# Kernel tuning notes

Measured on AMD Instinct MI355X. Metric: run time of the kernel, lower is better.

Reference implementation:

```python
import jax, jax.numpy as jnp
import numpy as np

N = 50000
K_CLASSES = 40
SIGMA = 0.2


def _lin(x, W, b):
    # x: [..., in], W: [out, in], b: [out]
    return x @ W.T + b


def setup_inputs() -> dict:
    key = jax.random.key(0)
    ks = iter(jax.random.split(key, 64))

    def rn(shape, scale=0.05):
        return jax.random.normal(next(ks), shape, dtype=jnp.float32) * scale

    inp = {
        "centre": jax.random.normal(next(ks), (N, 3), dtype=jnp.float32),
        "corner": jax.random.normal(next(ks), (N, 9), dtype=jnp.float32),
        "normal": jax.random.normal(next(ks), (N, 3), dtype=jnp.float32),
        "neighbour": jax.random.randint(next(ks), (N, 3), 0, N, dtype=jnp.int64 if jax.config.read('jax_enable_x64') else jnp.int32),
        # spatial_Des: linear2 (3->64), linear1 (64->64)
        "W_sp2": rn((64, 3)), "b_sp2": rn((64,)),
        "W_sp1": rn((64, 64)), "b_sp1": rn((64,)),
        # Face_Rotate_Conv: Conv1d(1,32,6,stride=3), linear3 (32->64), linear4 (64->64)
        "conv_w": rn((32, 1, 6)), "conv_b": rn((32,)),
        "W_fr3": rn((64, 32)), "b_fr3": rn((64,)),
        "W_fr4": rn((64, 64)), "b_fr4": rn((64,)),
        # Kernel_Correlation learned angles
        "theta": jax.random.uniform(next(ks), (1, 64, 4), dtype=jnp.float32) * np.pi,
        "phi": jax.random.uniform(next(ks), (1, 64, 4), dtype=jnp.float32) * 2 * np.pi,
        # Mesh1
        "W_c1": rn((256, 195)), "b_c1": rn((256,)),
        "W_a1": rn((256, 131)), "b_a1": rn((256,)),
        # Mesh2
        "W_c2": rn((512, 512)), "b_c2": rn((512,)),
        "W_a2": rn((512, 256)), "b_a2": rn((512,)),
        # fusion (1024->1024)
        "W_f": rn((1024, 1024)), "b_f": rn((1024,)),
        # mlp2 (1792->1024)
        "W_m2": rn((1024, 1792)), "b_m2": rn((1024,)),
        # mlp3 (1024->512->256->k), dropout in eval mode (identity)
        "W_m31": rn((512, 1024)), "b_m31": rn((512,)),
        "W_m32": rn((256, 512)), "b_m32": rn((256,)),
        "W_m33": rn((K_CLASSES, 256)), "b_m33": rn((K_CLASSES,)),
    }
    return inp


def reference(centre, corner, normal, neighbour,
              W_sp2, b_sp2, W_sp1, b_sp1,
              conv_w, conv_b, W_fr3, b_fr3, W_fr4, b_fr4,
              theta, phi,
              W_c1, b_c1, W_a1, b_a1,
              W_c2, b_c2, W_a2, b_a2,
              W_f, b_f, W_m2, b_m2,
              W_m31, b_m31, W_m32, b_m32, W_m33, b_m33):
    relu = jax.nn.relu
    nb0, nb1, nb2 = neighbour[:, 0], neighbour[:, 1], neighbour[:, 2]

    # ---- spatial descriptor: linear1(relu(linear2(centre))) -> [n,64]
    spatial = _lin(relu(_lin(centre, W_sp2, b_sp2)), W_sp1, b_sp1)

    # ---- Face_Rotate_Conv -> [n,64]
    x12 = jnp.concatenate([corner, corner[:, 0:3]], axis=1)          # [n,12]
    windows = jnp.stack([x12[:, 0:6], x12[:, 3:9], x12[:, 6:12]], 1)  # [n,3,6] (stride-3, k=6 conv windows)
    co = jnp.einsum('ntk,ok->nto', windows, conv_w[:, 0, :]) + conv_b  # [n,3,32]
    frc = _lin(relu(_lin(co.mean(axis=1), W_fr3, b_fr3)), W_fr4, b_fr4)  # [n,64]

    # ---- Kernel_Correlation -> [n,64]
    N4 = jnp.stack([normal, normal[nb0], normal[nb1], normal[nb2]], axis=1)  # [n,4,3]
    Kker = jnp.concatenate([jnp.sin(theta) * jnp.sin(phi),
                            jnp.sin(theta) * jnp.cos(phi),
                            jnp.cos(theta)], axis=0)                  # [3,64,4]
    Kt = jnp.transpose(Kker, (1, 2, 0))                               # [64,4,3]
    diff = N4[:, None, :, None, :] - Kt[None, :, None, :, :]          # [n,64,4,4,3]
    correl = jnp.sum(diff ** 2, axis=-1)                              # [n,64,4,4]
    kc = jnp.sum(jnp.exp(correl / (-2.0 * SIGMA ** 2)), axis=(2, 3)) / 16.0  # [n,64]

    # ---- structural descriptor -> [n,131]
    structural = jnp.concatenate([frc, kc, normal], axis=1)

    # ---- Mesh1: combination (195->256), aggregation (131->256)
    out1 = _lin(jnp.concatenate([spatial, structural], axis=1), W_c1, b_c1)
    agg1 = (structural + structural[nb0] + structural[nb1] + structural[nb2]) * 0.25
    out2 = _lin(agg1, W_a1, b_a1)

    # ---- Mesh2: combination (512->512), aggregation (256->512)
    out3 = _lin(jnp.concatenate([out1, out2], axis=1), W_c2, b_c2)
    agg2 = (out2 + out2[nb0] + out2[nb1] + out2[nb2]) * 0.25
    out4 = _lin(agg2, W_a2, b_a2)

    # ---- fusion + concat mlp + global max pool + classifier head
    fused = _lin(jnp.concatenate([out3, out4], axis=1), W_f, b_f)     # [n,1024]
    fea = jnp.concatenate([out1, out3, fused], axis=1)                # [n,1792]
    g = jnp.max(_lin(fea, W_m2, b_m2), axis=0)                        # [1024]
    h = relu(_lin(g, W_m31, b_m31))
    h = relu(_lin(h, W_m32, b_m32))
    logits = _lin(h, W_m33, b_m33)[None, :]                           # [1,k]
    return logits


if __name__ == '__main__':
    out = reference(**setup_inputs())
    print(out.shape)
```

## Files before the change

kernel.cpp:

```cpp
#include <hip/hip_runtime.h>
#include <hip/hip_bf16.h>
#include <stdint.h>

#define NPTS 50000
#define NPAD 50048

typedef unsigned short u16;
typedef __attribute__((ext_vector_type(8))) __bf16 bf16x8;
typedef __attribute__((ext_vector_type(4))) float f32x4;

__device__ __forceinline__ float bf2f(__hip_bfloat16 v) { return __bfloat162float(v); }
__device__ __forceinline__ __hip_bfloat16 f2bf(float v) { return __float2bfloat16(v); }
__device__ __forceinline__ float bfbits2f(unsigned short u) { return __uint_as_float(((unsigned)u) << 16); }
__device__ __forceinline__ unsigned short f2bfbits(float f) {
    __hip_bfloat16 h = f2bf(f);
    return *(unsigned short*)&h;
}
__device__ __forceinline__ int clampi(int v) { return v < 0 ? 0 : (v >= NPTS ? NPTS - 1 : v); }

__device__ __forceinline__ unsigned enc_f32(float f) {
    unsigned b = __float_as_uint(f);
    return (b & 0x80000000u) ? ~b : (b | 0x80000000u);
}
__device__ __forceinline__ float dec_f32(unsigned u) {
    return (u & 0x80000000u) ? __uint_as_float(u & 0x7fffffffu) : __uint_as_float(~u);
}

__device__ __forceinline__ void gload_lds16(const void* g, void* l) {
    __builtin_amdgcn_global_load_lds((__attribute__((address_space(1))) void*)g,
                                     (__attribute__((address_space(3))) void*)l, 16, 0, 0);
}

__device__ __forceinline__ ushort4 avg4(ushort4 a, ushort4 b, ushort4 c, ushort4 d) {
    ushort4 r;
    r.x = f2bfbits((bfbits2f(a.x) + bfbits2f(b.x) + bfbits2f(c.x) + bfbits2f(d.x)) * 0.25f);
    r.y = f2bfbits((bfbits2f(a.y) + bfbits2f(b.y) + bfbits2f(c.y) + bfbits2f(d.y)) * 0.25f);
    r.z = f2bfbits((bfbits2f(a.z) + bfbits2f(b.z) + bfbits2f(c.z) + bfbits2f(d.z)) * 0.25f);
    r.w = f2bfbits((bfbits2f(a.w) + bfbits2f(b.w) + bfbits2f(c.w) + bfbits2f(d.w)) * 0.25f);
    return r;
}

__device__ __forceinline__ void wg_body(
    const float* A, int lda, const float* B, int ldb,
    const float* D, int ldd, int dcols,
    float* Cf, __hip_bfloat16* Cb, int ldc, int K, int ncols, int zf,
    int bj, int bi, int t, float (*sA)[68], float (*sB)[68])
{
    const int tx = t & 15, ty = t >> 4;
    float acc[4][4] = {};
    for (int k0 = 0; k0 < K; k0 += 16) {
        {
            int k = t & 15, m = t >> 4;
#pragma unroll
            for (int q = 0; q < 4; ++q)
                sA[k][m + q * 16] = A[(long)(bi * 64 + m + q * 16) * lda + k0 + k];
            int n = t & 63, kk = t >> 6;
#pragma unroll
            for (int q = 0; q < 4; ++q)
                sB[kk + q * 4][n] = B[(long)(k0 + kk + q * 4) * ldb + bj * 64 + n];
        }
        __syncthreads();
#pragma unroll
        for (int k = 0; k < 16; ++k) {
            f32x4 av = *(const f32x4*)&sA[k][ty * 4];
            f32x4 bv = *(const f32x4*)&sB[k][tx * 4];
#pragma unroll
            for (int i = 0; i < 4; ++i)
#pragma unroll
                for (int j = 0; j < 4; ++j)
                    acc[i][j] += av[i] * bv[j];
        }
        __syncthreads();
    }
#pragma unroll
    for (int i = 0; i < 4; ++i) {
        int r = bi * 64 + ty * 4 + i;
#pragma unroll
        for (int j = 0; j < 4; ++j) {
            int cidx = bj * 64 + tx * 4 + j;
            if (cidx >= ncols) {
                if (zf && Cb) Cb[(long)r * ldc + cidx] = f2bf(0.f);
                continue;
            }
            float v = acc[i][j];
            if (D && cidx < dcols) v += D[(long)r * ldd + cidx];
            if (Cf) Cf[(long)r * ldc + cidx] = v;
            if (Cb) Cb[(long)r * ldc + cidx] = f2bf(v);
        }
    }
}

__device__ __forceinline__ void gather1_body4(
    const __hip_bfloat16* cat1, const int* neighbour, __hip_bfloat16* agg1,
    long pbase, int lane)
{
    if (lane >= 40) return;
    ushort4 va[4], vb[4], vc[4], vd[4];
#pragma unroll
    for (int q = 0; q < 4; ++q) {
        long p = pbase + q;
        if (p < NPTS) {
            int nb0 = clampi(neighbour[p * 3]), nb1 = clampi(neighbour[p * 3 + 1]), nb2 = clampi(neighbour[p * 3 + 2]);
            va[q] = ((const ushort4*)(cat1 + p * 224 + 64))[lane];
            vb[q] = ((const ushort4*)(cat1 + (long)nb0 * 224 + 64))[lane];
            vc[q] = ((const ushort4*)(cat1 + (long)nb1 * 224 + 64))[lane];
            vd[q] = ((const ushort4*)(cat1 + (long)nb2 * 224 + 64))[lane];
        }
    }
#pragma unroll
    for (int q = 0; q < 4; ++q) {
        long p = pbase + q;
        if (p >= NPAD) continue;
        ushort4* o = (ushort4*)(agg1 + p * 160);
        o[lane] = (p < NPTS) ? avg4(va[q], vb[q], vc[q], vd[q]) : make_ushort4(0, 0, 0, 0);
    }
}

__device__ __forceinline__ void gather1t_body4(
    const __hip_bfloat16* agg1, const int* neighbour, __hip_bfloat16* agg1t,
    long pbase, int lane)
{
    if (lane >= 48) return;
    if (lane >= 40) {
#pragma unroll
        for (int q = 0; q < 4; ++q) {
            long p = pbase + q;
            if (p < NPAD) ((ushort4*)(agg1t + p * 192))[lane] = make_ushort4(0, 0, 0, 0);
        }
        return;
    }
    ushort4 va[4], vb[4], vc[4], vd[4];
#pragma unroll
    for (int q = 0; q < 4; ++q) {
        long p = pbase + q;
        if (p < NPTS) {
            int nb0 = clampi(neighbour[p * 3]), nb1 = clampi(neighbour[p * 3 + 1]), nb2 = clampi(neighbour[p * 3 + 2]);
            va[q] = ((const ushort4*)(agg1 + p * 160))[lane];
            vb[q] = ((const ushort4*)(agg1 + (long)nb0 * 160))[lane];
            vc[q] = ((const ushort4*)(agg1 + (long)nb1 * 160))[lane];
            vd[q] = ((const ushort4*)(agg1 + (long)nb2 * 160))[lane];
        }
    }
#pragma unroll
    for (int q = 0; q < 4; ++q) {
        long p = pbase + q;
        if (p >= NPAD) continue;
        ushort4* o = (ushort4*)(agg1t + p * 192);
        o[lane] = (p < NPTS) ? avg4(va[q], vb[q], vc[q], vd[q]) : make_ushort4(0, 0, 0, 0);
    }
}

__device__ void featurize_body(
    const float* centre, const float* corner, const float* normal,
    const int* neighbour,
    const float* W_sp2, const float* b_sp2, const float* conv_w, const float* conv_b,
    const float* W_fr3, const float* b_fr3, const float* theta, const float* phi,
    __hip_bfloat16* cat1, int bid, int nblocks)
{
    __shared__ float sWsp2t[3][64];  __shared__ float sbsp2[64];
    __shared__ float sconvt[6][32];  __shared__ float sconvb[32];
    __shared__ float sWfr3t[32][64]; __shared__ float sbfr3[64];
    __shared__ float kt4x[4][64], kt4y[4][64], kt4z[4][64];

    const int tid = threadIdx.x;
    for (int i = tid; i < 2048; i += 256) { int j = i >> 5, k = i & 31; sWfr3t[k][j] = W_fr3[i]; }
    for (int i = tid; i < 192; i += 256) { int j = i / 3, k = i % 3; sWsp2t[k][j] = W_sp2[i]; }
    for (int i = tid; i < 192; i += 256) { int o = i / 6, k = i % 6; sconvt[k][o] = conv_w[i]; }
    if (tid < 64) { sbsp2[tid] = b_sp2[tid]; sbfr3[tid] = b_fr3[tid]; }
    if (tid < 32) sconvb[tid] = conv_b[tid];
    {
        int j = tid >> 2, s = tid & 3;
        float th = theta[tid], ph = phi[tid];
        float st = sinf(th), ct = cosf(th), sp = sinf(ph), cp = cosf(ph);
        kt4x[s][j] = st * sp; kt4y[s][j] = st * cp; kt4z[s][j] = ct;
    }
    __syncthreads();

    const int lane = tid & 63, wave = tid >> 6;
    for (long p = (long)bid * 4 + wave; p < NPAD; p += (long)nblocks * 4) {
        __hip_bfloat16* row = cat1 + p * 224;
        if (p >= NPTS) {
            __hip_bfloat16 z = f2bf(0.f);
            row[lane] = z; row[64 + lane] = z; row[128 + lane] = z;
            if (lane < 32) row[192 + lane] = z;
            continue;
        }
        float cx = centre[p * 3], cy = centre[p * 3 + 1], cz = centre[p * 3 + 2];
        float h1r = fmaxf(sbsp2[lane] + cx * sWsp2t[0][lane] + cy * sWsp2t[1][lane]
                          + cz * sWsp2t[2][lane], 0.f);
        float mval = 0.f;
        if (lane < 32) {
            float c0 = corner[p*9+0], c1 = corner[p*9+1], c2 = corner[p*9+2];
            float c3 = corner[p*9+3], c4 = corner[p*9+4], c5 = corner[p*9+5];
            float c6 = corner[p*9+6], c7 = corner[p*9+7], c8 = corner[p*9+8];
            float s0 = c0 + c3 + c6, s1 = c1 + c4 + c7, s2 = c2 + c5 + c8;
            mval = sconvb[lane] + (1.f / 3.f) *
                ((sconvt[0][lane] + sconvt[3][lane]) * s0 +
                 (sconvt[1][lane] + sconvt[4][lane]) * s1 +
                 (sconvt[2][lane] + sconvt[5][lane]) * s2);
        }
        float h3 = sbfr3[lane];
#pragma unroll 8
        for (int k = 0; k < 32; ++k) h3 += __shfl(mval, k) * sWfr3t[k][lane];
        float h3r = fmaxf(h3, 0.f);
        int nb0 = clampi(neighbour[p * 3]), nb1 = clampi(neighbour[p * 3 + 1]), nb2 = clampi(neighbour[p * 3 + 2]);
        float nx[4], ny[4], nz[4];
        nx[0] = normal[p * 3];          ny[0] = normal[p * 3 + 1];          nz[0] = normal[p * 3 + 2];
        nx[1] = normal[(long)nb0 * 3];  ny[1] = normal[(long)nb0 * 3 + 1];  nz[1] = normal[(long)nb0 * 3 + 2];
        nx[2] = normal[(long)nb1 * 3];  ny[2] = normal[(long)nb1 * 3 + 1];  nz[2] = normal[(long)nb1 * 3 + 2];
        nx[3] = normal[(long)nb2 * 3];  ny[3] = normal[(long)nb2 * 3 + 1];  nz[3] = normal[(long)nb2 * 3 + 2];
        float kcs = 0.f;
#pragma unroll
        for (int s = 0; s < 4; ++s) {
            float kx = kt4x[s][lane], ky = kt4y[s][lane], kz = kt4z[s][lane];
#pragma unroll
            for (int t = 0; t < 4; ++t) {
                float dx = nx[t] - kx, dy = ny[t] - ky, dz = nz[t] - kz;
                kcs += __expf(-12.5f * (dx * dx + dy * dy + dz * dz));
            }
        }
        float kcv = kcs * (1.f / 16.f);
        row[lane] = f2bf(h1r); row[64 + lane] = f2bf(h3r); row[128 + lane] = f2bf(kcv);
        if (lane < 32) {
            float nrmv = (lane == 0) ? nx[0] : (lane == 1) ? ny[0] : (lane == 2) ? nz[0] : 0.f;
            row[192 + lane] = f2bf(nrmv);
        }
    }
}

__global__ __launch_bounds__(256) void combo1(
    const float* __restrict__ W_c1, const float* __restrict__ W_a1,
    const float* __restrict__ W_sp1, const float* __restrict__ W_fr4,
    const float* __restrict__ W_f,
    const float* __restrict__ b_sp1, const float* __restrict__ b_fr4,
    const float* __restrict__ b_c1, const float* __restrict__ b_a1,
    const float* __restrict__ b_f, const float* __restrict__ b_a2,
    float* __restrict__ Wc1ff, float* __restrict__ Wa1ff,
    float* __restrict__ bc1v, float* __restrict__ b_a1p, float* __restrict__ w2,
    unsigned* __restrict__ g_enc,
    const float* __restrict__ centre, const float* __restrict__ corner,
    const float* __restrict__ normal, const int* __restrict__ neighbour,
    const float* __restrict__ W_sp2, const float* __restrict__ b_sp2,
    const float* __restrict__ conv_w, const float* __restrict__ conv_b,
    const float* __restrict__ W_fr3, const float* __restrict__ b_fr3,
    const float* __restrict__ theta, const float* __restrict__ phi,
    __hip_bfloat16* __restrict__ cat1)
{
    const int b = blockIdx.x, t = threadIdx.x;
    if (b >= 644) {
        featurize_body(centre, corner, normal, neighbour, W_sp2, b_sp2,
                       conv_w, conv_b, W_fr3, b_fr3, theta, phi, cat1, b - 644, 2048);
        return;
    }
    if (b < 256) {
        const int r = b;
        float vc, va;
        if (t < 64) {
            float s = 0.f;
            for (int k = 0; k < 64; ++k) s += W_c1[r * 195 + k] * W_sp1[k * 64 + t];
            vc = s;
            s = 0.f;
            for (int k = 0; k < 64; ++k) s += W_a1[r * 131 + k] * W_fr4[k * 64 + t];
            va = s;
        } else if (t < 128) {
            float s = 0.f;
            for (int k = 0; k < 64; ++k) s += W_c1[r * 195 + 64 + k] * W_fr4[k * 64 + (t - 64)];
            vc = s;
            va = W_a1[r * 131 + t];
        } else {
            vc = (t < 195) ? W_c1[r * 195 + t] : 0.f;
            va = (t < 131) ? W_a1[r * 131 + t] : 0.f;
        }
        Wc1ff[r * 256 + t] = vc;
        Wa1ff[r * 256 + t] = va;
    } else if (b < 640) {
        int o = (b - 256) * 4 + (t >> 6);
        int lane = t & 63;
        float a = 0.f;
        if (o < 256) {
            a = W_c1[o * 195 + lane] * b_sp1[lane] + W_c1[o * 195 + 64 + lane] * b_fr4[lane];
        } else if (o < 512) {
            a = W_a1[(o - 256) * 131 + lane] * b_fr4[lane];
        } else {
            for (int k = lane; k < 512; k += 64) a += W_f[(long)(o - 512) * 1024 + 512 + k] * b_a2[k];
        }
#pragma unroll
        for (int off = 32; off > 0; off >>= 1) a += __shfl_xor(a, off);
        if (lane == 0) {
            if (o < 256)      bc1v[o] = b_c1[o] + a;
            else if (o < 512) b_a1p[o - 256] = b_a1[o - 256] + a;
            else              w2[o - 512] = b_f[o - 512] + a;
        }
    } else {
        g_enc[(b - 640) * 256 + t] = 0x007FFFFFu;
    }
}

__global__ __launch_bounds__(256) void combo2(
    const float* __restrict__ W_m2, const float* __restrict__ W_f,
    const float* __restrict__ W_a2,
    float* __restrict__ T3f, float* __restrict__ B2f,
    const __hip_bfloat16* __restrict__ cat1, const int* __restrict__ neighbour,
    __hip_bfloat16* __restrict__ agg1)
{
    const int id = blockIdx.x, t = threadIdx.x;
    if (id < 192) {
        __shared__ float sA[16][68], sB[16][68];
        int bj = id % 12, bi = id / 12;
        if (bj < 8)
            wg_body(W_m2 + 768, 1792, W_f, 1024, W_m2 + 256, 1792, 512,
                    T3f, (__hip_bfloat16*)nullptr, 512, 1024, 512, 0, bj, bi, t, sA, sB);
        else
            wg_body(W_f + 512, 1024, W_a2, 256, (const float*)nullptr, 0, 0,
                    B2f, (__hip_bfloat16*)nullptr, 256, 512, 256, 0, bj - 8, bi, t, sA, sB);
    } else {
        long pbase = (long)(id - 192) * 16 + (t >> 6) * 4;
        gather1_body4(cat1, neighbour, agg1, pbase, t & 63);
    }
}

__global__ __launch_bounds__(256) void combo3(
    const float* __restrict__ T3f, const float* __restrict__ W_c2,
    const float* __restrict__ W_m2, const float* __restrict__ B2f,
    float* __restrict__ Uf, float* __restrict__ Vf,
    const __hip_bfloat16* __restrict__ agg1, const int* __restrict__ neighbour,
    __hip_bfloat16* __restrict__ agg1t)
{
    const int id = blockIdx.x, t = threadIdx.x;
    if (id < 192) {
        __shared__ float sA[16][68], sB[16][68];
        int bj = id % 12, bi = id / 12;
        if (bj < 8)
            wg_body(T3f, 512, W_c2, 512, W_m2, 1792, 256,
                    Uf, (__hip_bfloat16*)nullptr, 512, 512, 512, 0, bj, bi, t, sA, sB);
        else
            wg_body(W_m2 + 768, 1792, B2f, 256, (const float*)nullptr, 0, 0,
                    Vf, (__hip_bfloat16*)nullptr, 256, 1024, 256, 0, bj - 8, bi, t, sA, sB);
    } else {
        long pbase = (long)(id - 192) * 16 + (t >> 6) * 4;
        gather1t_body4(agg1, neighbour, agg1t, pbase, t & 63);
    }
}

__global__ __launch_bounds__(256) void l4(
    const float* __restrict__ Uf, const float* __restrict__ Vf,
    const float* __restrict__ Wc1ff, const float* __restrict__ Wa1ff,
    __hip_bfloat16* __restrict__ Xw,
    const float* __restrict__ W_m2, const float* __restrict__ T3f,
    const float* __restrict__ w2, const float* __restrict__ b_c2,
    const float* __restrict__ bc1v, const float* __restrict__ b_a1p,
    float* __restrict__ cvec,
    const __hip_bfloat16* __restrict__ agg1, const int* __restrict__ neighbour,
    __hip_bfloat16* __restrict__ agg1t)
{
    const int id = blockIdx.x, t = threadIdx.x;
    if (id >= 416) {
        long pbase = 32768 + (long)(id - 416) * 16 + (t >> 6) * 4;
        gather1t_body4(agg1, neighbour, agg1t, pbase, t & 63);
        return;
    }
    __shared__ float sA[16][68], sB[16][68];
    const int bx = id % 26, bi = id / 26;
    if (bx < 4) {
        wg_body(Uf, 512, Wc1ff, 256, (const float*)nullptr, 0, 0,
                (float*)nullptr, Xw, 576, 256, 224, 0, bx, bi, t, sA, sB);
    } else if (bx < 7) {
        wg_body(Uf + 256, 512, Wa1ff, 256, (const float*)nullptr, 0, 0,
                (float*)nullptr, Xw + 224, 576, 256, 160, 0, bx - 4, bi, t, sA, sB);
    } else if (bx < 10) {
        wg_body(Vf, 256, Wa1ff, 256, (const float*)nullptr, 0, 0,
                (float*)nullptr, Xw + 384, 576, 256, 160, 1, bx - 7, bi, t, sA, sB);
    } else {
        int i = ((bx - 10) * 16 + bi) * 4 + (t >> 6);
        int lane = t & 63;
        const float* m3row = W_m2 + (long)i * 1792 + 768;
        float a = 0.f;
        for (int k = lane; k < 1024; k += 64) a += w2[k] * m3row[k];
        for (int k = lane; k < 512;  k += 64) a += b_c2[k] * T3f[(long)i * 512 + k];
        for (int k = lane; k < 256;  k += 64) a += bc1v[k] * Uf[(long)i * 512 + k];
        for (int k = lane; k < 256;  k += 64) a += b_a1p[k] * Uf[(long)i * 512 + 256 + k];
        for (int k = lane; k < 256;  k += 64) a += b_a1p[k] * Vf[(long)i * 256 + k];
#pragma unroll
        for (int off = 32; off > 0; off >>= 1) a += __shfl_xor(a, off);
        if (lane == 0) cvec[i] = a;
    }
}

__global__ __launch_bounds__(256) void gemm_nt_max576(
    const __hip_bfloat16* __restrict__ A0,
    const __hip_bfloat16* __restrict__ A1,
    const __hip_bfloat16* __restrict__ A2,
    const __hip_bfloat16* __restrict__ B,
    unsigned* __restrict__ g_enc)
{
    __shared__ __align__(16) u16 Asm[2 * 128 * 32];
    __shared__ __align__(16) u16 Bsm[2 * 128 * 32];
    __shared__ float red[2][128];
    const int id = blockIdx.x;
    const int c = id & 7, tt = id >> 3;
    const int j8 = tt & 7, rh = tt >> 3;
    const int r = rh * 8 + c;
    if (r >= NPAD / 128) return;
    const long rowbase = (long)r * 128;
    const int colbase = j8 * 128;
    const int tid = threadIdx.x;
    const int lane = tid & 63, wave = tid >> 6;
    const int wr = wave >> 1, wc = wave & 1;
    const int m16 = lane & 15, kg = lane >> 4;
    const int srow = tid >> 2, skc = tid & 3;
    f32x4 acc[4][4] = {};
#pragma unroll
    for (int kt = 0; kt < 576; kt += 64) {
#pragma unroll
        for (int h = 0; h < 2; ++h) {
            const int kh = kt + h * 32;
#pragma unroll
            for (int i = 0; i < 2; ++i) {
                const int cid = i * 256 + tid;
                const int row = srow + i * 64, kc = skc;
                const __hip_bfloat16* Ap; long lda; int kl;
                if (kh < 224)      { Ap = A0; lda = 224; kl = kh; }
                else if (kh < 384) { Ap = A1; lda = 160; kl = kh - 224; }
                else               { Ap = A2; lda = 192; kl = kh - 384; }
                gload_lds16(Ap + (rowbase + row) * lda + kl + kc * 8, Asm + h * 4096 + cid * 8);
                gload_lds16(B + (long)(colbase + row) * 576 + kh + kc * 8, Bsm + h * 4096 + cid * 8);
            }
        }
        __syncthreads();
#pragma unroll
        for (int h = 0; h < 2; ++h) {
            bf16x8 af[4], bv[4];
#pragma unroll
            for (int i = 0; i < 4; ++i)
                af[i] = *(const bf16x8*)(Asm + h * 4096 + ((wr * 64 + i * 16 + m16) * 32 + kg * 8));
#pragma unroll
            for (int j = 0; j < 4; ++j)
                bv[j] = *(const bf16x8*)(Bsm + h * 4096 + ((wc * 64 + j * 16 + m16) * 32 + kg * 8));
#pragma unroll
            for (int i = 0; i < 4; ++i)
#pragma unroll
                for (int j = 0; j < 4; ++j)
                    acc[i][j] = __builtin_amdgcn_mfma_f32_16x16x32_bf16(af[i], bv[j], acc[i][j], 0, 0, 0);
        }
        __syncthreads();
    }
    const int q = lane >> 4;
#pragma unroll
    for (int j = 0; j < 4; ++j) {
        float m = -INFINITY;
#pragma unroll
        for (int i = 0; i < 4; ++i)
#pragma unroll
            for (int rr = 0; rr < 4; ++rr) {
                long rowg = rowbase + wr * 64 + i * 16 + q * 4 + rr;
                m = (rowg < NPTS) ? fmaxf(m, acc[i][j][rr]) : m;
            }
        m = fmaxf(m, __shfl_xor(m, 16));
        m = fmaxf(m, __shfl_xor(m, 32));
        if (lane < 16) red[wr][wc * 64 + j * 16 + m16] = m;
    }
    __syncthreads();
    if (tid < 128) {
        float v = fmaxf(red[0][tid], red[1][tid]);
        atomicMax(g_enc + colbase + tid, enc_f32(v));
    }
}

__global__ __launch_bounds__(256) void head_lin_g(
    const unsigned* __restrict__ g_enc, const float* __restrict__ cvec,
    const float* __restrict__ b_m2,
    const float* __restrict__ W, const float* __restrict__ b,
    float* __restrict__ out)
{
    int o = blockIdx.x * 4 + (threadIdx.x >> 6);
    int lane = threadIdx.x & 63;
    if (o >= 512) return;
    float a = 0.f;
    for (int k = lane; k < 1024; k += 64) {
        float g = dec_f32(g_enc[k]) + cvec[k] + b_m2[k];
        a += g * W[(long)o * 1024 + k];
    }
#pragma unroll
    for (int off = 32; off > 0; off >>= 1) a += __shfl_xor(a, off);
    if (lane == 0) out[o] = fmaxf(a + b[o], 0.f);
}

__global__ __launch_bounds__(256) void head_lin(
    const float* __restrict__ in, const float* __restrict__ W,
    const float* __restrict__ b, float* __restrict__ out,
    int In, int Out, int do_relu)
{
    int o = blockIdx.x * 4 + (threadIdx.x >> 6);
    int lane = threadIdx.x & 63;
    if (o >= Out) return;
    float a = 0.f;
    for (int k = lane; k < In; k += 64) a += in[k] * W[(long)o * In + k];
#pragma unroll
    for (int off = 32; off > 0; off >>= 1) a += __shfl_xor(a, off);
    if (lane == 0) {
        float v = a + b[o];
        out[o] = do_relu ? fmaxf(v, 0.f) : v;
    }
}

extern "C" void kernel_launch(void* const* d_in, const int* in_sizes, int n_in,
                              void* d_out, int out_size, void* d_ws, size_t ws_size,
                              hipStream_t stream)
{
    (void)in_sizes; (void)n_in; (void)out_size; (void)ws_size;
    const float* centre = (const float*)d_in[0];
    const float* corner = (const float*)d_in[1];
    const float* normal = (const float*)d_in[2];
    const int*   neighbour = (const int*)d_in[3];
    const float* W_sp2 = (const float*)d_in[4];
    const float* b_sp2 = (const float*)d_in[5];
    const float* W_sp1 = (const float*)d_in[6];
    const float* b_sp1 = (const float*)d_in[7];
    const float* conv_w = (const float*)d_in[8];
    const float* conv_b = (const float*)d_in[9];
    const float* W_fr3 = (const float*)d_in[10];
    const float* b_fr3 = (const float*)d_in[11];
    const float* W_fr4 = (const float*)d_in[12];
    const float* b_fr4 = (const float*)d_in[13];
    const float* theta = (const float*)d_in[14];
    const float* phi   = (const float*)d_in[15];
    const float* W_c1 = (const float*)d_in[16];
    const float* b_c1 = (const float*)d_in[17];
    const float* W_a1 = (const float*)d_in[18];
    const float* b_a1 = (const float*)d_in[19];
    const float* W_c2 = (const float*)d_in[20];
    const float* b_c2 = (const float*)d_in[21];
    const float* W_a2 = (const float*)d_in[22];
    const float* b_a2 = (const float*)d_in[23];
    const float* W_f  = (const float*)d_in[24];
    const float* b_f  = (const float*)d_in[25];
    const float* W_m2 = (const float*)d_in[26];
    const float* b_m2 = (const float*)d_in[27];
    const float* W_m31 = (const float*)d_in[28];
    const float* b_m31 = (const float*)d_in[29];
    const float* W_m32 = (const float*)d_in[30];
    const float* b_m32 = (const float*)d_in[31];
    const float* W_m33 = (const float*)d_in[32];
    const float* b_m33 = (const float*)d_in[33];

    char* ws = (char*)d_ws;
    size_t off = 0;
    auto alloc = [&](size_t bytes) { void* p = ws + off; off += (bytes + 255) & ~(size_t)255; return p; };
    __hip_bfloat16* cat1  = (__hip_bfloat16*)alloc((size_t)NPAD * 224 * 2);
    __hip_bfloat16* agg1  = (__hip_bfloat16*)alloc((size_t)NPAD * 160 * 2);
    __hip_bfloat16* agg1t = (__hip_bfloat16*)alloc((size_t)NPAD * 192 * 2);
    float* Wc1ff = (float*)alloc((size_t)65536 * 4);
    float* Wa1ff = (float*)alloc((size_t)65536 * 4);
    __hip_bfloat16* Xw = (__hip_bfloat16*)alloc((size_t)1024 * 576 * 2);
    float* T3f  = (float*)alloc((size_t)1024 * 512 * 4);
    float* Uf   = (float*)alloc((size_t)1024 * 512 * 4);
    float* B2f  = (float*)alloc((size_t)1024 * 256 * 4);
    float* Vf   = (float*)alloc((size_t)1024 * 256 * 4);
    float* bc1v = (float*)alloc(256 * 4);
    float* b_a1p = (float*)alloc(256 * 4);
    float* w2   = (float*)alloc(1024 * 4);
    float* cvec = (float*)alloc(1024 * 4);
    unsigned* g_enc = (unsigned*)alloc(1024 * 4);
    float* h1   = (float*)alloc(512 * 4);
    float* h2   = (float*)alloc(256 * 4);

    combo1<<<2692, 256, 0, stream>>>(W_c1, W_a1, W_sp1, W_fr4, W_f,
        b_sp1, b_fr4, b_c1, b_a1, b_f, b_a2,
        Wc1ff, Wa1ff, bc1v, b_a1p, w2, g_enc,
        centre, corner, normal, neighbour, W_sp2, b_sp2,
        conv_w, conv_b, W_fr3, b_fr3, theta, phi, cat1);
    combo2<<<192 + NPAD / 16, 256, 0, stream>>>(W_m2, W_f, W_a2, T3f, B2f,
        cat1, neighbour, agg1);
    combo3<<<192 + 2048, 256, 0, stream>>>(T3f, W_c2, W_m2, B2f, Uf, Vf,
        agg1, neighbour, agg1t);
    l4<<<416 + 1080, 256, 0, stream>>>(Uf, Vf, Wc1ff, Wa1ff, Xw,
        W_m2, T3f, w2, b_c2, bc1v, b_a1p, cvec,
        agg1, neighbour, agg1t);
    gemm_nt_max576<<<3136, 256, 0, stream>>>(cat1, agg1, agg1t, Xw, g_enc);
    head_lin_g<<<128, 256, 0, stream>>>(g_enc, cvec, b_m2, W_m31, b_m31, h1);
    head_lin<<<64, 256, 0, stream>>>(h1, W_m32, b_m32, h2, 512, 256, 1);
    head_lin<<<10, 256, 0, stream>>>(h2, W_m33, b_m33, (float*)d_out, 256, 40, 0);
}
```

Baseline: 390.7 us.

## Fuse second-hop neighbour aggregation into final GEMM A-tile load

The second aggregation buffer agg1t is no longer materialised. The final max-GEMM computes the 4-way neighbour average of agg1 on the fly while staging A tiles, and trims K from 576 to 544 (160 real columns instead of 192 padded). The first aggregation (agg1) is now split evenly across the three preceding combo kernels, which previously handled both hops. This removes a full write and read of the intermediate buffer and one kernel's worth of gather work, but adds gathered, non-async loads and averaging arithmetic inside the GEMM main loop, which may stall its pipeline.

After: 420.3 us. 7.6% more time.

```diff
diff --git a/kernel.cpp b/kernel.cpp
--- a/kernel.cpp
+++ b/kernel.cpp
@@ -38,6 +38,12 @@
     r.z = f2bfbits((bfbits2f(a.z) + bfbits2f(b.z) + bfbits2f(c.z) + bfbits2f(d.z)) * 0.25f);
     r.w = f2bfbits((bfbits2f(a.w) + bfbits2f(b.w) + bfbits2f(c.w) + bfbits2f(d.w)) * 0.25f);
     return r;
+}
+
+__device__ __forceinline__ unsigned avgpair(unsigned a, unsigned b, unsigned c, unsigned d) {
+    float lo = (bfbits2f(a & 0xffff) + bfbits2f(b & 0xffff) + bfbits2f(c & 0xffff) + bfbits2f(d & 0xffff)) * 0.25f;
+    float hi = (bfbits2f(a >> 16) + bfbits2f(b >> 16) + bfbits2f(c >> 16) + bfbits2f(d >> 16)) * 0.25f;
+    return (unsigned)f2bfbits(lo) | ((unsigned)f2bfbits(hi) << 16);
 }
 
 __device__ __forceinline__ void wg_body(
@@ -112,40 +118,6 @@
         long p = pbase + q;
         if (p >= NPAD) continue;
         ushort4* o = (ushort4*)(agg1 + p * 160);
-        o[lane] = (p < NPTS) ? avg4(va[q], vb[q], vc[q], vd[q]) : make_ushort4(0, 0, 0, 0);
-    }
-}
-
-__device__ __forceinline__ void gather1t_body4(
-    const __hip_bfloat16* agg1, const int* neighbour, __hip_bfloat16* agg1t,
-    long pbase, int lane)
-{
-    if (lane >= 48) return;
-    if (lane >= 40) {
-#pragma unroll
-        for (int q = 0; q < 4; ++q) {
-            long p = pbase + q;
-            if (p < NPAD) ((ushort4*)(agg1t + p * 192))[lane] = make_ushort4(0, 0, 0, 0);
-        }
-        return;
-    }
-    ushort4 va[4], vb[4], vc[4], vd[4];
-#pragma unroll
-    for (int q = 0; q < 4; ++q) {
-        long p = pbase + q;
-        if (p < NPTS) {
-            int nb0 = clampi(neighbour[p * 3]), nb1 = clampi(neighbour[p * 3 + 1]), nb2 = clampi(neighbour[p * 3 + 2]);
-            va[q] = ((const ushort4*)(agg1 + p * 160))[lane];
-            vb[q] = ((const ushort4*)(agg1 + (long)nb0 * 160))[lane];
-            vc[q] = ((const ushort4*)(agg1 + (long)nb1 * 160))[lane];
-            vd[q] = ((const ushort4*)(agg1 + (long)nb2 * 160))[lane];
-        }
-    }
-#pragma unroll
-    for (int q = 0; q < 4; ++q) {
-        long p = pbase + q;
-        if (p >= NPAD) continue;
-        ushort4* o = (ushort4*)(agg1t + p * 192);
         o[lane] = (p < NPTS) ? avg4(va[q], vb[q], vc[q], vd[q]) : make_ushort4(0, 0, 0, 0);
     }
 }
@@ -301,7 +273,7 @@
     const float* __restrict__ W_a2,
     float* __restrict__ T3f, float* __restrict__ B2f,
     const __hip_bfloat16* __restrict__ cat1, const int* __restrict__ neighbour,
-    __hip_bfloat16* __restrict__ agg1)
+    __hip_bfloat16* __restrict__ agg1, long p0)
 {
     const int id = blockIdx.x, t = threadIdx.x;
     if (id < 192) {
@@ -314,7 +286,7 @@
             wg_body(W_f + 512, 1024, W_a2, 256, (const float*)nullptr, 0, 0,
                     B2f, (__hip_bfloat16*)nullptr, 256, 512, 256, 0, bj - 8, bi, t, sA, sB);
     } else {
-        long pbase = (long)(id - 192) * 16 + (t >> 6) * 4;
+        long pbase = p0 + (long)(id - 192) * 16 + (t >> 6) * 4;
         gather1_body4(cat1, neighbour, agg1, pbase, t & 63);
     }
 }
@@ -323,8 +295,8 @@
     const float* __restrict__ T3f, const float* __restrict__ W_c2,
     const float* __restrict__ W_m2, const float* __restrict__ B2f,
     float* __restrict__ Uf, float* __restrict__ Vf,
-    const __hip_bfloat16* __restrict__ agg1, const int* __restrict__ neighbour,
-    __hip_bfloat16* __restrict__ agg1t)
+    const __hip_bfloat16* __restrict__ cat1, const int* __restrict__ neighbour,
+    __hip_bfloat16* __restrict__ agg1, long p0)
 {
     const int id = blockIdx.x, t = threadIdx.x;
     if (id < 192) {
@@ -337,8 +309,8 @@
             wg_body(W_m2 + 768, 1792, B2f, 256, (const float*)nullptr, 0, 0,
                     Vf, (__hip_bfloat16*)nullptr, 256, 1024, 256, 0, bj - 8, bi, t, sA, sB);
     } else {
-        long pbase = (long)(id - 192) * 16 + (t >> 6) * 4;
-        gather1t_body4(agg1, neighbour, agg1t, pbase, t & 63);
+        long pbase = p0 + (long)(id - 192) * 16 + (t >> 6) * 4;
+        gather1_body4(cat1, neighbour, agg1, pbase, t & 63);
     }
 }
 
@@ -350,13 +322,13 @@
     const float* __restrict__ w2, const float* __restrict__ b_c2,
     const float* __restrict__ bc1v, const float* __restrict__ b_a1p,
     float* __restrict__ cvec,
-    const __hip_bfloat16* __restrict__ agg1, const int* __restrict__ neighbour,
-    __hip_bfloat16* __restrict__ agg1t)
+    const __hip_bfloat16* __restrict__ cat1, const int* __restrict__ neighbour,
+    __hip_bfloat16* __restrict__ agg1, long p0)
 {
     const int id = blockIdx.x, t = threadIdx.x;
     if (id >= 416) {
-        long pbase = 32768 + (long)(id - 416) * 16 + (t >> 6) * 4;
-        gather1t_body4(agg1, neighbour, agg1t, pbase, t & 63);
+        long pbase = p0 + (long)(id - 416) * 16 + (t >> 6) * 4;
+        gather1_body4(cat1, neighbour, agg1, pbase, t & 63);
         return;
     }
     __shared__ float sA[16][68], sB[16][68];
@@ -369,7 +341,7 @@
                 (float*)nullptr, Xw + 224, 576, 256, 160, 0, bx - 4, bi, t, sA, sB);
     } else if (bx < 10) {
         wg_body(Vf, 256, Wa1ff, 256, (const float*)nullptr, 0, 0,
-                (float*)nullptr, Xw + 384, 576, 256, 160, 1, bx - 7, bi, t, sA, sB);
+                (float*)nullptr, Xw + 384, 576, 256, 160, 0, bx - 7, bi, t, sA, sB);
     } else {
         int i = ((bx - 10) * 16 + bi) * 4 + (t >> 6);
         int lane = t & 63;
@@ -386,10 +358,10 @@
     }
 }
 
-__global__ __launch_bounds__(256) void gemm_nt_max576(
+__global__ __launch_bounds__(256) void gemm_nt_max544(
     const __hip_bfloat16* __restrict__ A0,
     const __hip_bfloat16* __restrict__ A1,
-    const __hip_bfloat16* __restrict__ A2,
+    const int* __restrict__ neighbour,
     const __hip_bfloat16* __restrict__ B,
     unsigned* __restrict__ g_enc)
 {
@@ -408,27 +380,60 @@
     const int wr = wave >> 1, wc = wave & 1;
     const int m16 = lane & 15, kg = lane >> 4;
     const int srow = tid >> 2, skc = tid & 3;
+    int nbi[2][3]; bool pval[2];
+#pragma unroll
+    for (int i = 0; i < 2; ++i) {
+        long p = rowbase + srow + i * 64;
+        pval[i] = (p < NPTS);
+        if (pval[i]) {
+            nbi[i][0] = clampi(neighbour[p * 3]);
+            nbi[i][1] = clampi(neighbour[p * 3 + 1]);
+            nbi[i][2] = clampi(neighbour[p * 3 + 2]);
+        } else {
+            nbi[i][0] = nbi[i][1] = nbi[i][2] = 0;
+        }
+    }
     f32x4 acc[4][4] = {};
 #pragma unroll
-    for (int kt = 0; kt < 576; kt += 64) {
+    for (int kt = 0; kt < 544; kt += 64) {
+        const int nh = (kt + 64 <= 544) ? 2 : 1;
 #pragma unroll
         for (int h = 0; h < 2; ++h) {
+            if (h >= nh) break;
             const int kh = kt + h * 32;
 #pragma unroll
             for (int i = 0; i < 2; ++i) {
                 const int cid = i * 256 + tid;
-                const int row = srow + i * 64, kc = skc;
-                const __hip_bfloat16* Ap; long lda; int kl;
-                if (kh < 224)      { Ap = A0; lda = 224; kl = kh; }
-                else if (kh < 384) { Ap = A1; lda = 160; kl = kh - 224; }
-                else               { Ap = A2; lda = 192; kl = kh - 384; }
-                gload_lds16(Ap + (rowbase + row) * lda + kl + kc * 8, Asm + h * 4096 + cid * 8);
-                gload_lds16(B + (long)(colbase + row) * 576 + kh + kc * 8, Bsm + h * 4096 + cid * 8);
+                const int row = srow + i * 64;
+                gload_lds16(B + (long)(colbase + row) * 576 + kh + skc * 8, Bsm + h * 4096 + cid * 8);
+                if (kh < 224) {
+                    gload_lds16(A0 + (rowbase + row) * 224 + kh + skc * 8, Asm + h * 4096 + cid * 8);
+                } else if (kh < 384) {
+                    gload_lds16(A1 + (rowbase + row) * 160 + (kh - 224) + skc * 8, Asm + h * 4096 + cid * 8);
+                } else {
+                    const int col = (kh - 384) + skc * 8;
+                    uint4 v;
+                    if (pval[i]) {
+                        long p = rowbase + row;
+                        uint4 a = *(const uint4*)(A1 + p * 160 + col);
+                        uint4 b = *(const uint4*)(A1 + (long)nbi[i][0] * 160 + col);
+                        uint4 cc = *(const uint4*)(A1 + (long)nbi[i][1] * 160 + col);
+                        uint4 d = *(const uint4*)(A1 + (long)nbi[i][2] * 160 + col);
+                        v.x = avgpair(a.x, b.x, cc.x, d.x);
+                        v.y = avgpair(a.y, b.y, cc.y, d.y);
+                        v.z = avgpair(a.z, b.z, cc.z, d.z);
+                        v.w = avgpair(a.w, b.w, cc.w, d.w);
+                    } else {
+                        v = make_uint4(0, 0, 0, 0);
+                    }
+                    *(uint4*)(Asm + h * 4096 + cid * 8) = v;
+                }
             }
         }
         __syncthreads();
 #pragma unroll
         for (int h = 0; h < 2; ++h) {
+            if (h >= nh) break;
             bf16x8 af[4], bv[4];
 #pragma unroll
             for (int i = 0; i < 4; ++i)
@@ -548,7 +553,6 @@
     auto alloc = [&](size_t bytes) { void* p = ws + off; off += (bytes + 255) & ~(size_t)255; return p; };
     __hip_bfloat16* cat1  = (__hip_bfloat16*)alloc((size_t)NPAD * 224 * 2);
     __hip_bfloat16* agg1  = (__hip_bfloat16*)alloc((size_t)NPAD * 160 * 2);
-    __hip_bfloat16* agg1t = (__hip_bfloat16*)alloc((size_t)NPAD * 192 * 2);
     float* Wc1ff = (float*)alloc((size_t)65536 * 4);
     float* Wa1ff = (float*)alloc((size_t)65536 * 4);
     __hip_bfloat16* Xw = (__hip_bfloat16*)alloc((size_t)1024 * 576 * 2);
@@ -569,14 +573,14 @@
         Wc1ff, Wa1ff, bc1v, b_a1p, w2, g_enc,
         centre, corner, normal, neighbour, W_sp2, b_sp2,
         conv_w, conv_b, W_fr3, b_fr3, theta, phi, cat1);
-    combo2<<<192 + NPAD / 16, 256, 0, stream>>>(W_m2, W_f, W_a2, T3f, B2f,
-        cat1, neighbour, agg1);
-    combo3<<<192 + 2048, 256, 0, stream>>>(T3f, W_c2, W_m2, B2f, Uf, Vf,
-        agg1, neighbour, agg1t);
-    l4<<<416 + 1080, 256, 0, stream>>>(Uf, Vf, Wc1ff, Wa1ff, Xw,
+    combo2<<<192 + 1043, 256, 0, stream>>>(W_m2, W_f, W_a2, T3f, B2f,
+        cat1, neighbour, agg1, 0L);
+    combo3<<<192 + 1043, 256, 0, stream>>>(T3f, W_c2, W_m2, B2f, Uf, Vf,
+        cat1, neighbour, agg1, 16688L);
+    l4<<<416 + 1043, 256, 0, stream>>>(Uf, Vf, Wc1ff, Wa1ff, Xw,
         W_m2, T3f, w2, b_c2, bc1v, b_a1p, cvec,
-        agg1, neighbour, agg1t);
-    gemm_nt_max576<<<3136, 256, 0, stream>>>(cat1, agg1, agg1t, Xw, g_enc);
+        cat1, neighbour, agg1, 33376L);
+    gemm_nt_max544<<<3136, 256, 0, stream>>>(cat1, agg1, neighbour, Xw, g_enc);
     head_lin_g<<<128, 256, 0, stream>>>(g_enc, cvec, b_m2, W_m31, b_m31, h1);
     head_lin<<<64, 256, 0, stream>>>(h1, W_m32, b_m32, h2, 512, 256, 1);
     head_lin<<<10, 256, 0, stream>>>(h2, W_m33, b_m33, (float*)d_out, 256, 40, 0);
```

## Regroup weight-folding GEMMs and gathers into three fused kernels

Applied to the files above, without the earlier changes.

Moves the first weight-product stage (T3f/B2f) into the featurize kernel and shifts each later weight GEMM stage one kernel earlier, so each weight GEMM co-runs with a whole gather pass. This removes one kernel launch and its barrier. The second-hop gather, previously split across two launches, now runs entirely in the third kernel. It relies on the weight-only GEMMs being independent of the per-point data so they can share launches, and it may unbalance how the per-point and weight blocks fill each launch.

Measured after the change: 346.0 us. 1.13x faster.

```diff
diff --git a/kernel.cpp b/kernel.cpp
--- a/kernel.cpp
+++ b/kernel.cpp
@@ -228,7 +228,7 @@
     }
 }
 
-__global__ __launch_bounds__(256) void combo1(
+__global__ __launch_bounds__(256) void mega1(
     const float* __restrict__ W_c1, const float* __restrict__ W_a1,
     const float* __restrict__ W_sp1, const float* __restrict__ W_fr4,
     const float* __restrict__ W_f,
@@ -238,6 +238,8 @@
     float* __restrict__ Wc1ff, float* __restrict__ Wa1ff,
     float* __restrict__ bc1v, float* __restrict__ b_a1p, float* __restrict__ w2,
     unsigned* __restrict__ g_enc,
+    const float* __restrict__ W_m2, const float* __restrict__ W_a2,
+    float* __restrict__ T3f, float* __restrict__ B2f,
     const float* __restrict__ centre, const float* __restrict__ corner,
     const float* __restrict__ normal, const int* __restrict__ neighbour,
     const float* __restrict__ W_sp2, const float* __restrict__ b_sp2,
@@ -247,9 +249,9 @@
     __hip_bfloat16* __restrict__ cat1)
 {
     const int b = blockIdx.x, t = threadIdx.x;
-    if (b >= 644) {
+    if (b >= 836) {
         featurize_body(centre, corner, normal, neighbour, W_sp2, b_sp2,
-                       conv_w, conv_b, W_fr3, b_fr3, theta, phi, cat1, b - 644, 2048);
+                       conv_w, conv_b, W_fr3, b_fr3, theta, phi, cat1, b - 836, 2048);
         return;
     }
     if (b < 256) {
@@ -291,40 +293,26 @@
             else if (o < 512) b_a1p[o - 256] = b_a1[o - 256] + a;
             else              w2[o - 512] = b_f[o - 512] + a;
         }
+    } else if (b < 644) {
+        g_enc[(b - 640) * 256 + t] = 0x007FFFFFu;
     } else {
-        g_enc[(b - 640) * 256 + t] = 0x007FFFFFu;
-    }
-}
-
-__global__ __launch_bounds__(256) void combo2(
-    const float* __restrict__ W_m2, const float* __restrict__ W_f,
-    const float* __restrict__ W_a2,
-    float* __restrict__ T3f, float* __restrict__ B2f,
-    const __hip_bfloat16* __restrict__ cat1, const int* __restrict__ neighbour,
-    __hip_bfloat16* __restrict__ agg1)
-{
-    const int id = blockIdx.x, t = threadIdx.x;
-    if (id < 192) {
         __shared__ float sA[16][68], sB[16][68];
-        int bj = id % 12, bi = id / 12;
+        int idx = b - 644, bj = idx % 12, bi = idx / 12;
         if (bj < 8)
             wg_body(W_m2 + 768, 1792, W_f, 1024, W_m2 + 256, 1792, 512,
                     T3f, (__hip_bfloat16*)nullptr, 512, 1024, 512, 0, bj, bi, t, sA, sB);
         else
             wg_body(W_f + 512, 1024, W_a2, 256, (const float*)nullptr, 0, 0,
                     B2f, (__hip_bfloat16*)nullptr, 256, 512, 256, 0, bj - 8, bi, t, sA, sB);
-    } else {
-        long pbase = (long)(id - 192) * 16 + (t >> 6) * 4;
-        gather1_body4(cat1, neighbour, agg1, pbase, t & 63);
-    }
-}
-
-__global__ __launch_bounds__(256) void combo3(
+    }
+}
+
+__global__ __launch_bounds__(256) void mega2(
     const float* __restrict__ T3f, const float* __restrict__ W_c2,
     const float* __restrict__ W_m2, const float* __restrict__ B2f,
     float* __restrict__ Uf, float* __restrict__ Vf,
-    const __hip_bfloat16* __restrict__ agg1, const int* __restrict__ neighbour,
-    __hip_bfloat16* __restrict__ agg1t)
+    const __hip_bfloat16* __restrict__ cat1, const int* __restrict__ neighbour,
+    __hip_bfloat16* __restrict__ agg1)
 {
     const int id = blockIdx.x, t = threadIdx.x;
     if (id < 192) {
@@ -338,11 +326,11 @@
                     Vf, (__hip_bfloat16*)nullptr, 256, 1024, 256, 0, bj - 8, bi, t, sA, sB);
     } else {
         long pbase = (long)(id - 192) * 16 + (t >> 6) * 4;
-        gather1t_body4(agg1, neighbour, agg1t, pbase, t & 63);
-    }
-}
-
-__global__ __launch_bounds__(256) void l4(
+        gather1_body4(cat1, neighbour, agg1, pbase, t & 63);
+    }
+}
+
+__global__ __launch_bounds__(256) void mega3(
     const float* __restrict__ Uf, const float* __restrict__ Vf,
     const float* __restrict__ Wc1ff, const float* __restrict__ Wa1ff,
     __hip_bfloat16* __restrict__ Xw,
@@ -355,7 +343,7 @@
 {
     const int id = blockIdx.x, t = threadIdx.x;
     if (id >= 416) {
-        long pbase = 32768 + (long)(id - 416) * 16 + (t >> 6) * 4;
+        long pbase = (long)(id - 416) * 16 + (t >> 6) * 4;
         gather1t_body4(agg1, neighbour, agg1t, pbase, t & 63);
         return;
     }
@@ -564,16 +552,15 @@
     float* h1   = (float*)alloc(512 * 4);
     float* h2   = (float*)alloc(256 * 4);
 
-    combo1<<<2692, 256, 0, stream>>>(W_c1, W_a1, W_sp1, W_fr4, W_f,
+    mega1<<<2884, 256, 0, stream>>>(W_c1, W_a1, W_sp1, W_fr4, W_f,
         b_sp1, b_fr4, b_c1, b_a1, b_f, b_a2,
         Wc1ff, Wa1ff, bc1v, b_a1p, w2, g_enc,
+        W_m2, W_a2, T3f, B2f,
         centre, corner, normal, neighbour, W_sp2, b_sp2,
         conv_w, conv_b, W_fr3, b_fr3, theta, phi, cat1);
-    combo2<<<192 + NPAD / 16, 256, 0, stream>>>(W_m2, W_f, W_a2, T3f, B2f,
+    mega2<<<192 + 3128, 256, 0, stream>>>(T3f, W_c2, W_m2, B2f, Uf, Vf,
         cat1, neighbour, agg1);
-    combo3<<<192 + 2048, 256, 0, stream>>>(T3f, W_c2, W_m2, B2f, Uf, Vf,
-        agg1, neighbour, agg1t);
-    l4<<<416 + 1080, 256, 0, stream>>>(Uf, Vf, Wc1ff, Wa1ff, Xw,
+    mega3<<<416 + 3128, 256, 0, stream>>>(Uf, Vf, Wc1ff, Wa1ff, Xw,
         W_m2, T3f, w2, b_c2, bc1v, b_a1p, cvec,
         agg1, neighbour, agg1t);
     gemm_nt_max576<<<3136, 256, 0, stream>>>(cat1, agg1, agg1t, Xw, g_enc);
```
